# Performance work log

Hardware: AMD Instinct MI355X
Metric: run time of the kernel (lower is better)

Reference implementation:

```python
import jax, jax.numpy as jnp
import numpy as np

B, N, E, H = 2, 2048, 1024, 16
HD = E // H  # head_dim = 64


def setup_inputs() -> dict:
    key = jax.random.key(0)
    k1, k2, k3, k4, k5 = jax.random.split(key, 5)
    x = jax.random.normal(k1, (B, N, E), dtype=jnp.float32)
    # per-head Linear(E, 3*HD): stacked weights [H, E, 3*HD] and biases [H, 3*HD]
    Wqkv = jax.random.normal(k2, (H, E, 3 * HD), dtype=jnp.float32) * (1.0 / np.sqrt(E))
    bqkv = jax.random.normal(k3, (H, 3 * HD), dtype=jnp.float32) * 0.01
    Wout = jax.random.normal(k4, (E, E), dtype=jnp.float32) * (1.0 / np.sqrt(E))
    bout = jax.random.normal(k5, (E,), dtype=jnp.float32) * 0.01
    return {"x": x, "Wqkv": Wqkv, "bqkv": bqkv, "Wout": Wout, "bout": bout}


def reference(x, Wqkv, bqkv, Wout, bout):
    # per-head QKV projection, vectorized over heads: [B, H, N, 3*HD]
    proj = jnp.einsum('bne,hef->bhnf', x, Wqkv) + bqkv[None, :, None, :]
    k, q, v = jnp.split(proj, 3, axis=-1)  # each [B, H, N, HD]
    # scores = q @ k^T / sqrt(HD): [B, H, N, N]
    scores = jnp.einsum('bhqd,bhkd->bhqk', q, k) / jnp.sqrt(jnp.asarray(HD, dtype=x.dtype))
    # causal mask (tril)
    causal = jnp.tril(jnp.ones((N, N), dtype=bool))
    scores = jnp.where(causal[None, None, :, :], scores, -jnp.inf)
    attn = jax.nn.softmax(scores, axis=-1)
    sa = jnp.einsum('bhqk,bhkd->bhqd', attn, v)  # [B, H, N, HD]
    # concat heads in order -> [B, N, E]
    sa = jnp.transpose(sa, (0, 2, 1, 3)).reshape(B, N, E)
    return sa @ Wout + bout
```

## Files before the change

### kernel.cpp

```cpp
#include <hip/hip_runtime.h>
#include <hip/hip_bf16.h>

#define Bz 2
#define Nn 2048
#define Ee 1024
#define Hh 16
#define HD 64

typedef unsigned short u16;
typedef unsigned int u32;

typedef __bf16 bf16x8 __attribute__((ext_vector_type(8)));
typedef float f32x4 __attribute__((ext_vector_type(4)));

#define QK_SCALE 0.18033688f

__device__ __forceinline__ float bf2f(u16 u) {
    u32 v = ((u32)u) << 16;
    return __builtin_bit_cast(float, v);
}
__device__ __forceinline__ u16 f2bf(float f) {
    u32 i = __builtin_bit_cast(u32, f);
    u32 r = (i + 0x7FFFu + ((i >> 16) & 1u)) >> 16;
    return (u16)r;
}
__device__ __forceinline__ u32 pack2(float a, float b) {
    return (u32)f2bf(a) | ((u32)f2bf(b) << 16);
}
__device__ __forceinline__ u32 pack2h(float a, float b) {
    u32 ua = __builtin_bit_cast(u32, a) + 0x8000u;
    u32 ub = __builtin_bit_cast(u32, b) + 0x8000u;
    return (ua >> 16) | (ub & 0xFFFF0000u);
}
__device__ __forceinline__ bf16x8 ld_frag(const u16* p) {
    return __builtin_bit_cast(bf16x8, *(const uint4*)p);
}
__device__ __forceinline__ f32x4 zero4() {
    f32x4 z; z[0]=0.f; z[1]=0.f; z[2]=0.f; z[3]=0.f; return z;
}

__device__ __forceinline__ void async_copy16(const u16* g, u16* l) {
    __builtin_amdgcn_global_load_lds(
        (const __attribute__((address_space(1))) u32*)g,
        (__attribute__((address_space(3))) u32*)l, 16, 0, 0);
}

__global__ void ws_diag(float* out, float code) { out[0] = code; }

__global__ __launch_bounds__(256) void convert_x(
    const float* __restrict__ x, u16* __restrict__ xbf)
{
    size_t idx = ((size_t)blockIdx.x * 256 + threadIdx.x) * 8;
    float4 f0 = *(const float4*)(x + idx);
    float4 f1 = *(const float4*)(x + idx + 4);
    uint4 pk;
    pk.x = pack2(f0.x, f0.y); pk.y = pack2(f0.z, f0.w);
    pk.z = pack2(f1.x, f1.y); pk.w = pack2(f1.z, f1.w);
    *(uint4*)(xbf + idx) = pk;
}

__global__ __launch_bounds__(256) void transpose_f32_bf16(
    const float* __restrict__ src, u16* __restrict__ dst, int R, int C)
{
    const int r0 = blockIdx.x * 64, c0 = blockIdx.y * 64;
    const size_t zoff = (size_t)blockIdx.z * R * C;
    src += zoff; dst += zoff;
    const int tid = threadIdx.x;

    __shared__ float T[64][65];
    {
        int tr = tid >> 2, tc = (tid & 3) * 16;
        const float* s = src + (size_t)(r0 + tr) * C + c0 + tc;
#pragma unroll
        for (int j = 0; j < 4; ++j) {
            float4 v = ((const float4*)s)[j];
            T[tr][tc + 4 * j + 0] = v.x; T[tr][tc + 4 * j + 1] = v.y;
            T[tr][tc + 4 * j + 2] = v.z; T[tr][tc + 4 * j + 3] = v.w;
        }
    }
    __syncthreads();
    {
        int cc = tid >> 2, rr = (tid & 3) * 16;
        u16* d = dst + (size_t)(c0 + cc) * R + r0 + rr;
        u32 w[8];
#pragma unroll
        for (int i = 0; i < 8; ++i)
            w[i] = pack2(T[rr + 2 * i][cc], T[rr + 2 * i + 1][cc]);
        *(uint4*)(d)     = make_uint4(w[0], w[1], w[2], w[3]);
        *(uint4*)(d + 8) = make_uint4(w[4], w[5], w[6], w[7]);
    }
}

__global__ __launch_bounds__(256) void transpose_v(
    const u16* __restrict__ src, u16* __restrict__ dst)
{
    const int n0 = blockIdx.x * 64;
    const size_t z = blockIdx.y;
    src += z * (size_t)Nn * HD;
    dst += z * (size_t)HD * Nn;
    const int tid = threadIdx.x;

    __shared__ u16 T[64][66];
    {
        int tr = tid >> 2, tc = (tid & 3) * 16;
        const u16* s = src + (size_t)(n0 + tr) * HD + tc;
        *(uint4*)&T[tr][tc]     = *(const uint4*)(s);
        *(uint4*)&T[tr][tc + 8] = *(const uint4*)(s + 8);
    }
    __syncthreads();
    {
        int cc = tid >> 2, rr = (tid & 3) * 16;
        u32 w[8];
#pragma unroll
        for (int i = 0; i < 8; ++i)
            w[i] = (u32)T[rr + 2 * i][cc] | ((u32)T[rr + 2 * i + 1][cc] << 16);
        u16* d = dst + (size_t)cc * Nn + n0 + rr;
        *(uint4*)(d)     = make_uint4(w[0], w[1], w[2], w[3]);
        *(uint4*)(d + 8) = make_uint4(w[4], w[5], w[6], w[7]);
    }
}

__global__ __launch_bounds__(256) void qkv_mfma(
    const u16* __restrict__ xbf, const u16* __restrict__ Wt,
    const float* __restrict__ bias,
    u16* __restrict__ kbuf, u16* __restrict__ qbuf, u16* __restrict__ vbuf)
{
    const int mt = blockIdx.x;
    const int h  = blockIdx.y;
    const int tid = threadIdx.x;
    const int lane = tid & 63, wid = tid >> 6;
    const int wy = wid >> 1, wx = wid & 1;
    const int quad = lane >> 4, l15 = lane & 15;

    __shared__ u16 As[128 * 64];
    __shared__ u16 Bs[192 * 64];

    f32x4 acc[4][6];
#pragma unroll
    for (int mi = 0; mi < 4; ++mi)
#pragma unroll
        for (int ni = 0; ni < 6; ++ni) acc[mi][ni] = zero4();

    const u16* xb = xbf + (size_t)mt * 128 * Ee;
    const u16* wtb = Wt + (size_t)h * 192 * 1024;

    const int arowl = lane >> 3;
    const int jj = (lane & 7) ^ arowl;

    for (int kb = 0; kb < 16; ++kb) {
        __syncthreads();
#pragma unroll
        for (int i = 0; i < 4; ++i) {
            int rbase = (wid * 4 + i) * 8;
            const u16* g = xb + (size_t)(rbase + arowl) * Ee + kb * 64 + jj * 8;
            async_copy16(g, &As[(wid * 4 + i) * 512]);
        }
#pragma unroll
        for (int i = 0; i < 6; ++i) {
            int rbase = (wid * 6 + i) * 8;
            const u16* g = wtb + (size_t)(rbase + arowl) * 1024 + kb * 64 + jj * 8;
            async_copy16(g, &Bs[(wid * 6 + i) * 512]);
        }
        __syncthreads();

#pragma unroll
        for (int kk0 = 0; kk0 < 2; ++kk0) {
            const int pos = ((kk0 * 4 + quad) ^ (l15 & 7)) * 8;
            bf16x8 af[4], bf[6];
#pragma unroll
            for (int mi = 0; mi < 4; ++mi)
                af[mi] = ld_frag(&As[(wy * 64 + mi * 16 + l15) * 64 + pos]);
#pragma unroll
            for (int ni = 0; ni < 6; ++ni)
                bf[ni] = ld_frag(&Bs[(wx * 96 + ni * 16 + l15) * 64 + pos]);
#pragma unroll
            for (int mi = 0; mi < 4; ++mi)
#pragma unroll
                for (int ni = 0; ni < 6; ++ni)
                    acc[mi][ni] = __builtin_amdgcn_mfma_f32_16x16x32_bf16(
                        af[mi], bf[ni], acc[mi][ni], 0, 0, 0);
        }
    }

#pragma unroll
    for (int ni = 0; ni < 6; ++ni) {
        int col = wx * 96 + ni * 16 + l15;
        int ft = col >> 6, d = col & 63;
        u16* dst = (ft == 0) ? kbuf : (ft == 1) ? qbuf : vbuf;
        float sc = (ft == 1) ? QK_SCALE : 1.0f;
        float bv = bias[h * 192 + col];
#pragma unroll
        for (int mi = 0; mi < 4; ++mi)
#pragma unroll
            for (int r = 0; r < 4; ++r) {
                int gm = mt * 128 + wy * 64 + mi * 16 + quad * 4 + r;
                int bb = gm >> 11, n = gm & (Nn - 1);
                dst[(((size_t)(bb * Hh + h)) * Nn + n) * HD + d] =
                    f2bf((acc[mi][ni][r] + bv) * sc);
            }
    }
}

__global__ __launch_bounds__(256) void attn2(
    const u16* __restrict__ qbuf, const u16* __restrict__ kbuf,
    const u16* __restrict__ vtb, u16* __restrict__ p0buf,
    u16* __restrict__ p1buf, float* __restrict__ ml)
{
    const int id = blockIdx.x;
    const int bh = (id & 7) * 4 + ((id >> 3) & 3);
    const int p  = id >> 5;
    const int tid = threadIdx.x;
    const int lane = tid & 63, wid = tid >> 6;
    const int l15 = lane & 15, quad = lane >> 4;

    __shared__ u16 KsL[2][4096];
    __shared__ u16 VtL[2][4096];

    const u16* qb = qbuf + (size_t)bh * Nn * HD;
    const u16* kb = kbuf + (size_t)bh * Nn * HD;
    const u16* vt = vtb + (size_t)bh * HD * Nn;

    const int r_l = lane >> 3;
    const int jj = (lane & 7) ^ r_l;
    const int xsw = l15 & 7;
    const int src0 = l15 + (quad & 1) * 32;
    const bool qhi = quad >= 2;

    for (int sg = 0; sg < 2; ++sg) {
        const int qt = sg ? (31 - p) : p;
        const int T  = qt + 1;
        const int t0 = sg ? ((T + 1) >> 1) : 0;
        const int t1 = sg ? T : ((p + 2) >> 1);
        u16*   pb = sg ? p1buf : p0buf;
        float* mb = ml + (sg ? 131072 : 0);
        float* lb = ml + (sg ? 196608 : 65536);

        const int qrow = qt * 64 + wid * 16 + l15;

        f32x4 oacc[4];
#pragma unroll
        for (int dt = 0; dt < 4; ++dt) oacc[dt] = zero4();
        float m_i = -3e38f, l_i = 0.f;

        if (t0 < t1) {
            bf16x8 qf[2];
#pragma unroll
            for (int st = 0; st < 2; ++st)
                qf[st] = __builtin_bit_cast(bf16x8,
                    *(const uint4*)(qb + (size_t)qrow * HD + st * 32 + quad * 8));

            __syncthreads();
#pragma unroll
            for (int i2 = 0; i2 < 4; ++i2) {
                int idx = wid * 4 + i2;
                if (idx < 8) {
                    const u16* g = kb + (size_t)(t0 * 64 + idx * 8 + r_l) * HD + jj * 8;
                    async_copy16(g, &KsL[0][idx * 512]);
                } else {
                    int ii = idx - 8;
                    const u16* g = vt + (size_t)(ii * 8 + r_l) * Nn + t0 * 64 + jj * 8;
                    async_copy16(g, &VtL[0][ii * 512]);
                }
            }

            const int nit = t1 - t0;
            for (int i = 0; i < nit; ++i) {
                const int tk = t0 + i;
                __syncthreads();
                if (i + 1 < nit) {
                    const int nb = (i + 1) & 1;
#pragma unroll
                    for (int i2 = 0; i2 < 4; ++i2) {
                        int idx = wid * 4 + i2;
                        if (idx < 8) {
                            const u16* g = kb + (size_t)((tk + 1) * 64 + idx * 8 + r_l) * HD + jj * 8;
                            async_copy16(g, &KsL[nb][idx * 512]);
                        } else {
                            int ii = idx - 8;
                            const u16* g = vt + (size_t)(ii * 8 + r_l) * Nn + (tk + 1) * 64 + jj * 8;
                            async_copy16(g, &VtL[nb][ii * 512]);
                        }
                    }
                }
                const u16* K = KsL[i & 1];
                const u16* V = VtL[i & 1];

                f32x4 s[4];
#pragma unroll
                for (int t = 0; t < 4; ++t) {
                    f32x4 a = zero4();
#pragma unroll
                    for (int st = 0; st < 2; ++st) {
                        bf16x8 kf = ld_frag(&K[(t * 16 + l15) * 64 +
                                               ((st * 4 + quad) ^ xsw) * 8]);
                        a = __builtin_amdgcn_mfma_f32_16x16x32_bf16(kf, qf[st], a, 0, 0, 0);
                    }
                    s[t] = a;
                }

                if (tk == qt) {
#pragma unroll
                    for (int t = 0; t < 4; ++t)
#pragma unroll
                        for (int r = 0; r < 4; ++r) {
                            int key = tk * 64 + t * 16 + quad * 4 + r;
                            if (key > qrow) s[t][r] = -3e38f;
                        }
                }

                float mx = s[0][0];
#pragma unroll
                for (int t = 0; t < 4; ++t)
#pragma unroll
                    for (int r = 0; r < 4; ++r) mx = fmaxf(mx, s[t][r]);
                mx = fmaxf(mx, __shfl_xor(mx, 16));
                mx = fmaxf(mx, __shfl_xor(mx, 32));
                float mn = fmaxf(m_i, mx);
                float alpha = exp2f(m_i - mn);
                m_i = mn;
                float rs = 0.f;
#pragma unroll
                for (int t = 0; t < 4; ++t)
#pragma unroll
                    for (int r = 0; r < 4; ++r) {
                        float e = exp2f(s[t][r] - mn);
                        s[t][r] = e;
                        rs += e;
                    }
                rs += __shfl_xor(rs, 16);
                rs += __shfl_xor(rs, 32);
                l_i = l_i * alpha + rs;
#pragma unroll
                for (int dt = 0; dt < 4; ++dt)
#pragma unroll
                    for (int r = 0; r < 4; ++r) oacc[dt][r] *= alpha;

                u32 pk[4][2];
#pragma unroll
                for (int t = 0; t < 4; ++t) {
                    pk[t][0] = pack2h(s[t][0], s[t][1]);
                    pk[t][1] = pack2h(s[t][2], s[t][3]);
                }
#pragma unroll
                for (int st = 0; st < 2; ++st) {
                    u32 e0 = pk[2 * st][0],     e1 = pk[2 * st][1];
                    u32 o0 = pk[2 * st + 1][0], o1 = pk[2 * st + 1][1];
                    u32 A0 = __shfl(e0, src0),      B0 = __shfl(o0, src0);
                    u32 A1 = __shfl(e1, src0),      B1 = __shfl(o1, src0);
                    u32 A2 = __shfl(e0, src0 + 16), B2 = __shfl(o0, src0 + 16);
                    u32 A3 = __shfl(e1, src0 + 16), B3 = __shfl(o1, src0 + 16);
                    u32 U0 = qhi ? B0 : A0;
                    u32 U1 = qhi ? B1 : A1;
                    u32 U2 = qhi ? B2 : A2;
                    u32 U3 = qhi ? B3 : A3;
                    bf16x8 pf = __builtin_bit_cast(bf16x8, make_uint4(U0, U1, U2, U3));
#pragma unroll
                    for (int dt = 0; dt < 4; ++dt) {
                        bf16x8 vf = ld_frag(&V[(dt * 16 + l15) * 64 +
                                               ((st * 4 + quad) ^ xsw) * 8]);
                        oacc[dt] = __builtin_amdgcn_mfma_f32_16x16x32_bf16(
                            vf, pf, oacc[dt], 0, 0, 0);
                    }
                }
            }
        }

#pragma unroll
        for (int dt = 0; dt < 4; ++dt) {
            ushort4 ov;
            ov.x = f2bf(oacc[dt][0]);
            ov.y = f2bf(oacc[dt][1]);
            ov.z = f2bf(oacc[dt][2]);
            ov.w = f2bf(oacc[dt][3]);
            *(ushort4*)&pb[((size_t)bh * Nn + qrow) * HD + dt * 16 + quad * 4] = ov;
        }
        if (quad == 0) {
            mb[bh * Nn + qrow] = m_i;
            lb[bh * Nn + qrow] = l_i;
        }
    }
}

__global__ __launch_bounds__(256) void attn_merge(
    const u16* __restrict__ p0, u16* __restrict__ p1,
    const float* __restrict__ ml)
{
    const int idx = blockIdx.x * 256 + threadIdx.x;
    const int row = idx >> 3;
    const int dc = (idx & 7) * 8;

    const float m1 = ml[row],          l1 = ml[65536 + row];
    const float m2 = ml[131072 + row], l2 = ml[196608 + row];
    const float m = fmaxf(m1, m2);
    const float a1 = exp2f(m1 - m), a2 = exp2f(m2 - m);
    const float inv = 1.f / (a1 * l1 + a2 * l2);
    const float s1 = a1 * inv, s2 = a2 * inv;

    const size_t off = (size_t)row * HD + dc;
    uint4 v0 = *(const uint4*)&p0[off];
    uint4 v1 = *(const uint4*)&p1[off];
    u32 a[4] = {v0.x, v0.y, v0.z, v0.w};
    u32 b[4] = {v1.x, v1.y, v1.z, v1.w};
    u32 w[4];
#pragma unroll
    for (int j = 0; j < 4; ++j) {
        float x0 = bf2f((u16)a[j]) * s1 + bf2f((u16)b[j]) * s2;
        float x1 = bf2f((u16)(a[j] >> 16)) * s1 + bf2f((u16)(b[j] >> 16)) * s2;
        w[j] = pack2(x0, x1);
    }
    *(uint4*)&p1[off] = make_uint4(w[0], w[1], w[2], w[3]);
}

typedef float f32x16 __attribute__((ext_vector_type(16)));
__device__ __forceinline__ f32x16 zero16() {
    f32x16 z;
#pragma unroll
    for (int i = 0; i < 16; ++i) z[i] = 0.f;
    return z;
}

__global__ __launch_bounds__(256) void out_mfma(
    const u16* __restrict__ A, const u16* __restrict__ Wt,
    const float* __restrict__ bias, float* __restrict__ out)
{
    const int mt = blockIdx.x;
    const int nt = blockIdx.y;
    const int tid = threadIdx.x;
    const int lane = tid & 63, wid = tid >> 6;
    const int l31 = lane & 31, khalf = (lane >> 5) * 8;

    __shared__ u16 As[128][72];
    __shared__ u16 Bs[64][72];

    f32x16 acc[2];
    acc[0] = zero16(); acc[1] = zero16();

    const int arow = tid >> 1, akh = (tid & 1) * 32;
    const int gm = mt * 128 + arow;
    const int bb = gm >> 11, n = gm & (Nn - 1);
    const int brow = tid >> 2, bc = (tid & 3) * 16;

    for (int k0 = 0; k0 < Ee; k0 += 64) {
        __syncthreads();
        {
            const int c = k0 + akh;
            const int h = c >> 6, d0 = c & 63;
            const u16* asrc = A + (((size_t)(bb * Hh + h) * Nn + n) * HD + d0);
#pragma unroll
            for (int j = 0; j < 4; ++j)
                *(uint4*)&As[arow][akh + 8 * j] = *(const uint4*)(asrc + 8 * j);
            const u16* bsrc = Wt + (size_t)(nt * 64 + brow) * 1024 + k0 + bc;
            *(uint4*)&Bs[brow][bc]     = *(const uint4*)(bsrc);
            *(uint4*)&Bs[brow][bc + 8] = *(const uint4*)(bsrc + 8);
        }
        __syncthreads();
#pragma unroll
        for (int kc = 0; kc < 4; ++kc) {
            bf16x8 af = ld_frag(&As[wid * 32 + l31][kc * 16 + khalf]);
#pragma unroll
            for (int ct = 0; ct < 2; ++ct) {
                bf16x8 bf = ld_frag(&Bs[ct * 32 + l31][kc * 16 + khalf]);
                acc[ct] = __builtin_amdgcn_mfma_f32_32x32x16_bf16(af, bf, acc[ct], 0, 0, 0);
            }
        }
    }

#pragma unroll
    for (int ct = 0; ct < 2; ++ct) {
        int col = nt * 64 + ct * 32 + l31;
        float bv = bias[col];
#pragma unroll
        for (int r = 0; r < 16; ++r) {
            int row_l = (r & 3) + 8 * (r >> 2) + 4 * (lane >> 5);
            int gm2 = mt * 128 + wid * 32 + row_l;
            out[(size_t)gm2 * Ee + col] = acc[ct][r] + bv;
        }
    }
}

extern "C" void kernel_launch(void* const* d_in, const int* in_sizes, int n_in,
                              void* d_out, int out_size, void* d_ws, size_t ws_size,
                              hipStream_t stream) {
    const float* x    = (const float*)d_in[0];
    const float* Wqkv = (const float*)d_in[1];
    const float* bqkv = (const float*)d_in[2];
    const float* Wout = (const float*)d_in[3];
    const float* bout = (const float*)d_in[4];
    float* out = (float*)d_out;

    const size_t SZ = (size_t)Bz * Hh * Nn * HD;
    const size_t NSA = (size_t)Bz * Nn * Ee;
    const size_t NEED = (3 * SZ + NSA) * sizeof(u16);

    if (ws_size < NEED) {
        ws_diag<<<1, 1, 0, stream>>>(out, 20000.0f + (float)(ws_size >> 20));
        return;
    }

    u16* ws = (u16*)d_ws;
    u16* kbuf  = ws;
    u16* qbuf  = ws + SZ;
    u16* vbuf  = ws + 2 * SZ;
    u16* sabuf = ws + 3 * SZ;
    u16* wqkv_t = sabuf;
    u16* wout_t = kbuf;
    u16* xbf    = (u16*)d_out;
    u16* vtb    = (u16*)d_out + SZ;
    u16* p0     = (u16*)d_out;
    u16* p1     = vbuf;
    float* ml   = (float*)sabuf;

    convert_x<<<2048, 256, 0, stream>>>(x, xbf);
    transpose_f32_bf16<<<dim3(16, 3, 16), 256, 0, stream>>>(Wqkv, wqkv_t, 1024, 192);
    qkv_mfma<<<dim3(32, 16), 256, 0, stream>>>(xbf, wqkv_t, bqkv, kbuf, qbuf, vbuf);
    transpose_v<<<dim3(32, 32), 256, 0, stream>>>(vbuf, vtb);
    attn2<<<dim3(1024), 256, 0, stream>>>(qbuf, kbuf, vtb, p0, p1, ml);
    attn_merge<<<dim3(2048), 256, 0, stream>>>(p0, p1, ml);
    transpose_f32_bf16<<<dim3(16, 16, 1), 256, 0, stream>>>(Wout, wout_t, 1024, 1024);
    out_mfma<<<dim3(32, 16), 256, 0, stream>>>(p1, wout_t, bout, out);
}
```

Baseline: 197.0 us.

## Use permlane swaps, hardware bf16 pack, and lazy softmax rescale in attention

Replaces the ds_bpermute-based shuffles for the row max/sum reductions and the P-fragment transpose with permlane16/32 swap instructions. It swaps the manual bf16 packing for the hardware v_cvt_pk_bf16_f32 instruction and uses the raw exp2 builtin. It also skips the running-max update and accumulator rescale unless some lane's new max exceeds the old max by more than 8 (a threshold in the exp2 domain). The aim is to cut LDS-crossbar traffic and VALU work in the softmax inner loop. The lazy rescale lets unnormalised exponentials grow up to 2^8 before the rescale, and the pack now rounds nearest-even instead of round-half-up.

```diff
diff --git a/kernel.cpp b/kernel.cpp
--- a/kernel.cpp
+++ b/kernel.cpp
@@ -12,6 +12,7 @@
 
 typedef __bf16 bf16x8 __attribute__((ext_vector_type(8)));
 typedef float f32x4 __attribute__((ext_vector_type(4)));
+typedef unsigned int u32x2 __attribute__((ext_vector_type(2)));
 
 #define QK_SCALE 0.18033688f
 
@@ -27,16 +28,43 @@
 __device__ __forceinline__ u32 pack2(float a, float b) {
     return (u32)f2bf(a) | ((u32)f2bf(b) << 16);
 }
-__device__ __forceinline__ u32 pack2h(float a, float b) {
-    u32 ua = __builtin_bit_cast(u32, a) + 0x8000u;
-    u32 ub = __builtin_bit_cast(u32, b) + 0x8000u;
-    return (ua >> 16) | (ub & 0xFFFF0000u);
-}
 __device__ __forceinline__ bf16x8 ld_frag(const u16* p) {
     return __builtin_bit_cast(bf16x8, *(const uint4*)p);
 }
 __device__ __forceinline__ f32x4 zero4() {
     f32x4 z; z[0]=0.f; z[1]=0.f; z[2]=0.f; z[3]=0.f; return z;
+}
+
+__device__ __forceinline__ u32 cvt_pk_bf16(float a, float b) {
+    u32 r;
+    asm("v_cvt_pk_bf16_f32 %0, %1, %2" : "=v"(r) : "v"(a), "v"(b));
+    return r;
+}
+__device__ __forceinline__ u32x2 pl32(u32 a, u32 b) {
+    return __builtin_amdgcn_permlane32_swap(a, b, false, false);
+}
+__device__ __forceinline__ u32x2 pl16(u32 a, u32 b) {
+    return __builtin_amdgcn_permlane16_swap(a, b, false, false);
+}
+__device__ __forceinline__ float qred_max(float x) {
+    u32 xu = __builtin_bit_cast(u32, x);
+    u32x2 r1 = pl16(xu, xu);
+    float m = fmaxf(__builtin_bit_cast(float, (u32)r1[0]),
+                    __builtin_bit_cast(float, (u32)r1[1]));
+    u32 mu = __builtin_bit_cast(u32, m);
+    u32x2 r2 = pl32(mu, mu);
+    return fmaxf(__builtin_bit_cast(float, (u32)r2[0]),
+                 __builtin_bit_cast(float, (u32)r2[1]));
+}
+__device__ __forceinline__ float qred_sum(float x) {
+    u32 xu = __builtin_bit_cast(u32, x);
+    u32x2 r1 = pl16(xu, xu);
+    float m = __builtin_bit_cast(float, (u32)r1[0]) +
+              __builtin_bit_cast(float, (u32)r1[1]);
+    u32 mu = __builtin_bit_cast(u32, m);
+    u32x2 r2 = pl32(mu, mu);
+    return __builtin_bit_cast(float, (u32)r2[0]) +
+           __builtin_bit_cast(float, (u32)r2[1]);
 }
 
 __device__ __forceinline__ void async_copy16(const u16* g, u16* l) {
@@ -223,8 +251,6 @@
     const int r_l = lane >> 3;
     const int jj = (lane & 7) ^ r_l;
     const int xsw = l15 & 7;
-    const int src0 = l15 + (quad & 1) * 32;
-    const bool qhi = quad >= 2;
 
     for (int sg = 0; sg < 2; ++sg) {
         const int qt = sg ? (31 - p) : p;
@@ -313,47 +339,42 @@
                 for (int t = 0; t < 4; ++t)
 #pragma unroll
                     for (int r = 0; r < 4; ++r) mx = fmaxf(mx, s[t][r]);
-                mx = fmaxf(mx, __shfl_xor(mx, 16));
-                mx = fmaxf(mx, __shfl_xor(mx, 32));
-                float mn = fmaxf(m_i, mx);
-                float alpha = exp2f(m_i - mn);
-                m_i = mn;
+                mx = qred_max(mx);
+                if (!__all(mx <= m_i + 8.0f)) {
+                    float mn = fmaxf(m_i, mx);
+                    float alpha = __builtin_amdgcn_exp2f(m_i - mn);
+                    m_i = mn;
+                    l_i *= alpha;
+#pragma unroll
+                    for (int dt = 0; dt < 4; ++dt)
+#pragma unroll
+                        for (int r = 0; r < 4; ++r) oacc[dt][r] *= alpha;
+                }
                 float rs = 0.f;
 #pragma unroll
                 for (int t = 0; t < 4; ++t)
 #pragma unroll
                     for (int r = 0; r < 4; ++r) {
-                        float e = exp2f(s[t][r] - mn);
+                        float e = __builtin_amdgcn_exp2f(s[t][r] - m_i);
                         s[t][r] = e;
                         rs += e;
                     }
-                rs += __shfl_xor(rs, 16);
-                rs += __shfl_xor(rs, 32);
-                l_i = l_i * alpha + rs;
-#pragma unroll
-                for (int dt = 0; dt < 4; ++dt)
-#pragma unroll
-                    for (int r = 0; r < 4; ++r) oacc[dt][r] *= alpha;
+                l_i += qred_sum(rs);
 
                 u32 pk[4][2];
 #pragma unroll
                 for (int t = 0; t < 4; ++t) {
-                    pk[t][0] = pack2h(s[t][0], s[t][1]);
-                    pk[t][1] = pack2h(s[t][2], s[t][3]);
+                    pk[t][0] = cvt_pk_bf16(s[t][0], s[t][1]);
+                    pk[t][1] = cvt_pk_bf16(s[t][2], s[t][3]);
                 }
 #pragma unroll
                 for (int st = 0; st < 2; ++st) {
-                    u32 e0 = pk[2 * st][0],     e1 = pk[2 * st][1];
-                    u32 o0 = pk[2 * st + 1][0], o1 = pk[2 * st + 1][1];
-                    u32 A0 = __shfl(e0, src0),      B0 = __shfl(o0, src0);
-                    u32 A1 = __shfl(e1, src0),      B1 = __shfl(o1, src0);
-                    u32 A2 = __shfl(e0, src0 + 16), B2 = __shfl(o0, src0 + 16);
-                    u32 A3 = __shfl(e1, src0 + 16), B3 = __shfl(o1, src0 + 16);
-                    u32 U0 = qhi ? B0 : A0;
-                    u32 U1 = qhi ? B1 : A1;
-                    u32 U2 = qhi ? B2 : A2;
-                    u32 U3 = qhi ? B3 : A3;
-                    bf16x8 pf = __builtin_bit_cast(bf16x8, make_uint4(U0, U1, U2, U3));
+                    u32x2 s0 = pl32(pk[2 * st][0], pk[2 * st + 1][0]);
+                    u32x2 u02 = pl16((u32)s0[0], (u32)s0[1]);
+                    u32x2 s1 = pl32(pk[2 * st][1], pk[2 * st + 1][1]);
+                    u32x2 u13 = pl16((u32)s1[0], (u32)s1[1]);
+                    bf16x8 pf = __builtin_bit_cast(bf16x8,
+                        make_uint4((u32)u02[0], (u32)u13[0], (u32)u02[1], (u32)u13[1]));
 #pragma unroll
                     for (int dt = 0; dt < 4; ++dt) {
                         bf16x8 vf = ld_frag(&V[(dt * 16 + l15) * 64 +
```

Result: faster. 184.3 us (-6.5%).
